# Kernel optimization log

Hardware: AMD Instinct MI355X
Metric: run time of the kernel (lower is better)

The kernel has to match this reference:

```python
import jax, jax.numpy as jnp
import numpy as np

T, N, D = 64, 40, 4
H, R, K = 256, 64, 2
E = N * (N - 1)


def _xavier(key, shape):
    std = (2.0 / (shape[0] + shape[1])) ** 0.5
    return (std * jax.random.normal(key, shape)).astype(jnp.float32)


def setup_inputs() -> dict:
    ks = iter(jax.random.split(jax.random.key(0), 40))
    send, recv = np.where(np.ones((N, N)) - np.eye(N))  # fully-connected directed graph, E = N*(N-1)
    p = {}
    p['inputs'] = jax.random.normal(next(ks), (1, T, N, D), dtype=jnp.float32)
    p['node_masks'] = jnp.ones((1, T, N), dtype=jnp.float32)
    p['send_edges'] = jnp.asarray(send, dtype=jnp.int32)
    p['recv_edges'] = jnp.asarray(recv, dtype=jnp.int32)
    for name, nin in (('mlp1', D), ('mlp2', 2 * H), ('mlp3', H), ('mlp4', 3 * H)):
        p[name + '_W1'] = _xavier(next(ks), (H, nin))
        p[name + '_b1'] = jnp.full((H,), 0.1, jnp.float32)
        p[name + '_W2'] = _xavier(next(ks), (H, H))
        p[name + '_b2'] = jnp.full((H,), 0.1, jnp.float32)
    s = float(1.0 / np.sqrt(R))
    for nm in ('fwd', 'rev'):
        p[nm + '_Wih'] = jax.random.uniform(next(ks), (4 * R, H), jnp.float32, -s, s)
        p[nm + '_Whh'] = jax.random.uniform(next(ks), (4 * R, R), jnp.float32, -s, s)
        p[nm + '_bih'] = jnp.zeros((4 * R,), jnp.float32)
        p[nm + '_bhh'] = jnp.zeros((4 * R,), jnp.float32)
    p['enc_W'] = _xavier(next(ks), (K, 2 * R))
    p['enc_b'] = jnp.full((K,), 0.1, jnp.float32)
    p['prior_W'] = _xavier(next(ks), (K, R))
    p['prior_b'] = jnp.full((K,), 0.1, jnp.float32)
    return p


def _mlp(x, W1, b1, W2, b2):
    # RefNRIMLP in eval mode with no_bn=True: elu(fc2(elu(fc1(x))))
    return jax.nn.elu(jax.nn.elu(x @ W1.T + b1) @ W2.T + b2)


def _lstm(xs, Wih, Whh, bih, bhh):
    # xs: [T, E, H] -> hidden states [T, E, R]; PyTorch LSTM gate order i, f, g, o
    def step(carry, xt):
        h, c = carry
        g = xt @ Wih.T + bih + h @ Whh.T + bhh
        i, f, gg, o = jnp.split(g, 4, axis=-1)
        c = jax.nn.sigmoid(f) * c + jax.nn.sigmoid(i) * jnp.tanh(gg)
        h = jax.nn.sigmoid(o) * jnp.tanh(c)
        return (h, c), h
    Rh = Whh.shape[1]
    init = (jnp.zeros((xs.shape[1], Rh), xs.dtype), jnp.zeros((xs.shape[1], Rh), xs.dtype))
    _, hs = jax.lax.scan(step, init, xs)
    return hs


def _encode(inputs, send, recv,
            m1W1, m1b1, m1W2, m1b2, m2W1, m2b1, m2W2, m2b2,
            m3W1, m3b1, m3W2, m3b2, m4W1, m4b1, m4W2, m4b2,
            fWih, fWhh, fbih, fbhh, rWih, rWhh, rbih, rbhh,
            encW, encb, priW, prib):
    x = inputs[0]                                                  # [T, N, D]
    h = _mlp(x, m1W1, m1b1, m1W2, m1b2)                            # [T, N, H]
    e = jnp.concatenate([h[:, send], h[:, recv]], axis=-1)         # node2edge gather [T, E, 2H]
    e = _mlp(e, m2W1, m2b1, m2W2, m2b2)                            # [T, E, H]
    skip = e
    n = jnp.zeros((x.shape[0], x.shape[1], e.shape[-1]), e.dtype)
    n = n.at[:, recv].add(e)                                       # edge2node scatter-add (index_add_)
    n = _mlp(n, m3W1, m3b1, m3W2, m3b2)                            # [T, N, H]
    e = jnp.concatenate([n[:, send], n[:, recv], skip], axis=-1)   # [T, E, 3H]
    e = _mlp(e, m4W1, m4b1, m4W2, m4b2)                            # per-edge features over time [T, E, H]
    fwd_h = _lstm(e, fWih, fWhh, fbih, fbhh)                       # [T, E, R]
    rev_h = _lstm(e[::-1], rWih, rWhh, rbih, rbhh)[::-1]           # [T, E, R]
    prior = fwd_h @ priW.T + prib                                  # [T, E, K]
    enc = jnp.concatenate([fwd_h, rev_h], axis=-1) @ encW.T + encb # [T, E, K]
    return jnp.concatenate([prior, enc], axis=-1)                  # [T, E, 2K]


def reference(inputs, node_masks, send_edges, recv_edges,
              mlp1_W1, mlp1_b1, mlp1_W2, mlp1_b2,
              mlp2_W1, mlp2_b1, mlp2_W2, mlp2_b2,
              mlp3_W1, mlp3_b1, mlp3_W2, mlp3_b2,
              mlp4_W1, mlp4_b1, mlp4_W2, mlp4_b2,
              fwd_Wih, fwd_Whh, fwd_bih, fwd_bhh,
              rev_Wih, rev_Whh, rev_bih, rev_bhh,
              enc_W, enc_b, prior_W, prior_b):
    del node_masks  # all nodes present -> static fully-connected graph each step
    return _encode(inputs, send_edges, recv_edges,
                   mlp1_W1, mlp1_b1, mlp1_W2, mlp1_b2,
                   mlp2_W1, mlp2_b1, mlp2_W2, mlp2_b2,
                   mlp3_W1, mlp3_b1, mlp3_W2, mlp3_b2,
                   mlp4_W1, mlp4_b1, mlp4_W2, mlp4_b2,
                   fwd_Wih, fwd_Whh, fwd_bih, fwd_bhh,
                   rev_Wih, rev_Whh, rev_bih, rev_bhh,
                   enc_W, enc_b, prior_W, prior_b)
```

## Files before the change

kernel.cpp:

```cpp
#include <hip/hip_runtime.h>
#include <math.h>

#define T_ 64
#define N_ 40
#define D_ 4
#define H_ 256
#define R_ 64
#define E_ 1560
#define TE_ (T_*E_)
#define TN_ (T_*N_)

typedef unsigned short us;
typedef short short8 __attribute__((ext_vector_type(8)));
typedef float f32x4 __attribute__((ext_vector_type(4)));

__device__ __forceinline__ float elu_f(float x){ return x > 0.f ? x : (__expf(x) - 1.f); }
__device__ __forceinline__ float sig_f(float x){ return 1.f/(1.f+__expf(-x)); }
__device__ __forceinline__ float tanh_f(float x){ return 2.f/(1.f+__expf(-2.f*x)) - 1.f; }
__device__ __forceinline__ float dot4(float4 a, float4 b){ return a.x*b.x + a.y*b.y + a.z*b.z + a.w*b.w; }

__device__ __forceinline__ float bf2f(us u){ return __uint_as_float(((unsigned int)u) << 16); }
__device__ __forceinline__ us f2bf(float f){
    unsigned int u = __float_as_uint(f);
    u += 0x7FFFu + ((u >> 16) & 1u);
    return (us)(u >> 16);
}
__device__ __forceinline__ float4 ld4f(const float* p){ return *(const float4*)p; }
__device__ __forceinline__ float4 ld4f(const us* p){
    ushort4 v = *(const ushort4*)p;
    return make_float4(bf2f(v.x), bf2f(v.y), bf2f(v.z), bf2f(v.w));
}
__device__ __forceinline__ void st4f(float* p, float4 v){ *(float4*)p = v; }
__device__ __forceinline__ void st4f(us* p, float4 v){
    ushort4 o; o.x = f2bf(v.x); o.y = f2bf(v.y); o.z = f2bf(v.z); o.w = f2bf(v.w);
    *(ushort4*)p = o;
}

__device__ __forceinline__ void gld16(void* lds, const void* g){
    __builtin_amdgcn_global_load_lds((const __attribute__((address_space(1))) unsigned int*)g,
                                     (__attribute__((address_space(3))) unsigned int*)lds,
                                     16, 0, 0);
}

__device__ __forceinline__ void wsplit1(const float* W, us* hi, us* lo, int i){
    const float w = W[i];
    const us h = f2bf(w);
    hi[i] = h;
    lo[i] = f2bf(w - bf2f(h));
}

__global__ __launch_bounds__(256)
void wsplit_all(const float* __restrict__ s0, us* h0, us* l0,
                const float* __restrict__ s1, us* h1, us* l1,
                const float* __restrict__ s2, us* h2, us* l2,
                const float* __restrict__ s3, us* h3, us* l3,
                const float* __restrict__ s4, us* h4, us* l4,
                const float* __restrict__ s5, us* h5, us* l5,
                const float* __restrict__ s6, us* h6, us* l6,
                const float* __restrict__ s7, us* h7, us* l7)
{
    int i = blockIdx.x * 256 + threadIdx.x;
    if (i < 131072) { wsplit1(s0, h0, l0, i); return; } i -= 131072;
    if (i <  65536) { wsplit1(s1, h1, l1, i); return; } i -=  65536;
    if (i < 196608) { wsplit1(s2, h2, l2, i); return; } i -= 196608;
    if (i <  65536) { wsplit1(s3, h3, l3, i); return; } i -=  65536;
    if (i <  65536) { wsplit1(s4, h4, l4, i); return; } i -=  65536;
    if (i <  65536) { wsplit1(s5, h5, l5, i); return; } i -=  65536;
    if (i <  16384) { wsplit1(s6, h6, l6, i); return; } i -=  16384;
    wsplit1(s7, h7, l7, i);
}

__global__ __launch_bounds__(256)
void mlp1_kernel(const float* __restrict__ x,
                 const float* __restrict__ W1, const float* __restrict__ b1,
                 const float* __restrict__ W2, const float* __restrict__ b2,
                 us* __restrict__ hout)
{
    __shared__ float xs[8][4];
    __shared__ float h1[8][256];
    const int tid = threadIdx.x;
    const int r0  = blockIdx.x * 8;

    if (tid < 32) xs[tid >> 2][tid & 3] = x[r0 * 4 + tid];
    __syncthreads();

    const float4 w1 = *(const float4*)&W1[tid * 4];
    const float bb1 = b1[tid];
    #pragma unroll
    for (int row = 0; row < 8; ++row) {
        float v = bb1 + xs[row][0]*w1.x + xs[row][1]*w1.y + xs[row][2]*w1.z + xs[row][3]*w1.w;
        h1[row][tid] = elu_f(v);
    }
    __syncthreads();

    float acc[8];
    const float bb2 = b2[tid];
    #pragma unroll
    for (int row = 0; row < 8; ++row) acc[row] = bb2;
    const float* w2row = W2 + (size_t)tid * 256;
    for (int k4 = 0; k4 < 64; ++k4) {
        const float4 w = *(const float4*)&w2row[k4 * 4];
        #pragma unroll
        for (int row = 0; row < 8; ++row) {
            const float4 hh = *(const float4*)&h1[row][k4 * 4];
            acc[row] += dot4(hh, w);
        }
    }
    #pragma unroll
    for (int row = 0; row < 8; ++row)
        hout[(size_t)(r0 + row) * 256 + tid] = f2bf(elu_f(acc[row]));
}

template<int MODE, bool DOELU>
__global__ __launch_bounds__(256)
void gemm_mfma(const us* __restrict__ A, const us* __restrict__ A2, const us* __restrict__ A3,
               const us* __restrict__ Whi, const us* __restrict__ Wlo,
               const float* __restrict__ bias1, const float* __restrict__ bias2,
               const int* __restrict__ send, const int* __restrict__ recv,
               us* __restrict__ C, int Kdim,
               const us* __restrict__ Whi2, const us* __restrict__ Wlo2,
               const float* __restrict__ bias1b, const float* __restrict__ bias2b,
               us* __restrict__ C2)
{
    __shared__ char smem[49152];

    const int tid  = threadIdx.x;
    const int lane = tid & 63;
    const int w    = tid >> 6;
    const int ml   = lane & 15;
    const int q    = lane >> 4;
    const int bx   = blockIdx.x;
    int by         = blockIdx.y;
    const int eh   = w >> 1;
    const int fh   = w & 1;

    if (MODE == 0 && C2 != nullptr && by >= 2) {
        Whi = Whi2; Wlo = Wlo2; bias1 = bias1b; bias2 = bias2b; C = C2; by -= 2;
    }

    const int srow0 = w * 32 + (lane >> 2);
    const int srow1 = srow0 + 16;
    const int cofs  = (((lane & 3) ^ ((lane >> 3) & 3)) * 8);

    const int gr0 = bx * 128 + srow0, gr1 = bx * 128 + srow1;
    const us *pA0a=nullptr,*pA1a=nullptr,*pA2a=nullptr;
    const us *pA0b=nullptr,*pA1b=nullptr,*pA2b=nullptr;
    if (MODE == 0) {
        pA0a = A + (size_t)gr0 * Kdim;
        pA0b = A + (size_t)gr1 * Kdim;
    } else {
        const int t0 = gr0 / E_, e0 = gr0 - t0 * E_;
        const int t1 = gr1 / E_, e1 = gr1 - t1 * E_;
        pA0a = A  + ((size_t)(t0 * N_ + send[e0])) * H_;
        pA1a = A2 + ((size_t)(t0 * N_ + recv[e0])) * H_;
        pA0b = A  + ((size_t)(t1 * N_ + send[e1])) * H_;
        pA1b = A2 + ((size_t)(t1 * N_ + recv[e1])) * H_;
        if (MODE == 2) { pA2a = A3 + (size_t)gr0 * H_; pA2b = A3 + (size_t)gr1 * H_; }
    }
    const us* pWh0 = Whi + (size_t)(by * 128 + srow0) * Kdim;
    const us* pWh1 = Whi + (size_t)(by * 128 + srow1) * Kdim;
    const us* pWl0 = Wlo + (size_t)(by * 128 + srow0) * Kdim;
    const us* pWl1 = Wlo + (size_t)(by * 128 + srow1) * Kdim;

    f32x4 acc[4][4];
    #pragma unroll
    for (int i = 0; i < 4; ++i)
        #pragma unroll
        for (int j = 0; j < 4; ++j)
            acc[i][j] = (f32x4){0.f, 0.f, 0.f, 0.f};

    auto stage = [&](int k0, char* base) {
        const us *sa, *sb;
        if (MODE == 0) { sa = pA0a + k0; sb = pA0b + k0; }
        else if (MODE == 1) {
            sa = (k0 < 256) ? pA0a + k0 : pA1a + (k0 - 256);
            sb = (k0 < 256) ? pA0b + k0 : pA1b + (k0 - 256);
        } else {
            sa = (k0 < 256) ? pA0a + k0 : (k0 < 512) ? pA1a + (k0 - 256) : pA2a + (k0 - 512);
            sb = (k0 < 256) ? pA0b + k0 : (k0 < 512) ? pA1b + (k0 - 256) : pA2b + (k0 - 512);
        }
        gld16(base + w * 2048,                sa + cofs);
        gld16(base + w * 2048 + 1024,         sb + cofs);
        gld16(base + 8192  + w * 2048,        pWh0 + k0 + cofs);
        gld16(base + 8192  + w * 2048 + 1024, pWh1 + k0 + cofs);
        gld16(base + 16384 + w * 2048,        pWl0 + k0 + cofs);
        gld16(base + 16384 + w * 2048 + 1024, pWl1 + k0 + cofs);
    };

    const int qs16 = (q ^ ((ml >> 1) & 3)) * 16;

    stage(0, smem);
    const int nk = Kdim >> 5;
    for (int k = 0; k < nk; ++k) {
        char* cur = smem + (k & 1) * 24576;
        char* nxt = smem + ((k + 1) & 1) * 24576;
        __builtin_amdgcn_s_barrier();
        if (k + 1 < nk) {
            stage((k + 1) * 32, nxt);
            __builtin_amdgcn_s_waitcnt(0x3F76);
        } else {
            __builtin_amdgcn_s_waitcnt(0x3F70);
        }
        __builtin_amdgcn_s_barrier();

        short8 wh[4], wl[4], ef[4];
        #pragma unroll
        for (int mt = 0; mt < 4; ++mt) {
            const int blkOf = (fh * 4 + mt) * 1024 + ml * 64 + qs16;
            wh[mt] = *(const short8*)(cur + 8192  + blkOf);
            wl[mt] = *(const short8*)(cur + 16384 + blkOf);
        }
        #pragma unroll
        for (int nt = 0; nt < 4; ++nt) {
            const int blkOf = (eh * 4 + nt) * 1024 + ml * 64 + qs16;
            ef[nt] = *(const short8*)(cur + blkOf);
        }
        #pragma unroll
        for (int mt = 0; mt < 4; ++mt)
            #pragma unroll
            for (int nt = 0; nt < 4; ++nt) {
                acc[mt][nt] = __builtin_amdgcn_mfma_f32_16x16x32_bf16(wh[mt], ef[nt], acc[mt][nt], 0, 0, 0);
                acc[mt][nt] = __builtin_amdgcn_mfma_f32_16x16x32_bf16(wl[mt], ef[nt], acc[mt][nt], 0, 0, 0);
            }
    }

    #pragma unroll
    for (int mt = 0; mt < 4; ++mt) {
        const int colb = by * 128 + fh * 64 + mt * 16 + q * 4;
        float4 bb = *(const float4*)(bias1 + colb);
        if (bias2) {
            const float4 b2 = *(const float4*)(bias2 + colb);
            bb.x += b2.x; bb.y += b2.y; bb.z += b2.z; bb.w += b2.w;
        }
        #pragma unroll
        for (int nt = 0; nt < 4; ++nt) {
            const int row = bx * 128 + eh * 64 + nt * 16 + ml;
            float4 v;
            v.x = acc[mt][nt][0] + bb.x; v.y = acc[mt][nt][1] + bb.y;
            v.z = acc[mt][nt][2] + bb.z; v.w = acc[mt][nt][3] + bb.w;
            if (DOELU) { v.x = elu_f(v.x); v.y = elu_f(v.y); v.z = elu_f(v.z); v.w = elu_f(v.w); }
            ushort4 o; o.x = f2bf(v.x); o.y = f2bf(v.y); o.z = f2bf(v.z); o.w = f2bf(v.w);
            *(ushort4*)(C + (size_t)row * 256 + colb) = o;
        }
    }
}

template<bool DOELU, typename TA, typename TC>
__global__ __launch_bounds__(256)
void gemm_nt(const TA* __restrict__ A, const float* __restrict__ W,
             const float* __restrict__ bias1,
             TC* __restrict__ C, int M, int Kdim)
{
    __shared__ float As[16][64];
    __shared__ float Ws[16][64];

    const int tid = threadIdx.x;
    const int am  = tid >> 2;
    const int ak  = (tid & 3) * 4;
    const int gm  = blockIdx.x * 64 + am;

    const TA* aptr0 = A + (size_t)gm * Kdim;
    const float* wptr = W + (size_t)(blockIdx.y * 64 + am) * Kdim;

    const int tx = tid & 15, ty = tid >> 4;
    float acc[4][4] = {};

    for (int k0 = 0; k0 < Kdim; k0 += 16) {
        const float4 a4 = ld4f(aptr0 + k0 + ak);
        const float4 w4 = *(const float4*)(wptr + k0 + (tid & 3) * 4);

        __syncthreads();
        As[ak+0][am] = a4.x; As[ak+1][am] = a4.y; As[ak+2][am] = a4.z; As[ak+3][am] = a4.w;
        const int wk = (tid & 3) * 4;
        Ws[wk+0][am] = w4.x; Ws[wk+1][am] = w4.y; Ws[wk+2][am] = w4.z; Ws[wk+3][am] = w4.w;
        __syncthreads();

        #pragma unroll
        for (int kq = 0; kq < 16; ++kq) {
            const float4 av = *(const float4*)&As[kq][ty * 4];
            const float4 wv = *(const float4*)&Ws[kq][tx * 4];
            const float a_[4] = {av.x, av.y, av.z, av.w};
            const float w_[4] = {wv.x, wv.y, wv.z, wv.w};
            #pragma unroll
            for (int i = 0; i < 4; ++i)
                #pragma unroll
                for (int j = 0; j < 4; ++j)
                    acc[i][j] += a_[i] * w_[j];
        }
    }

    const int gn = blockIdx.y * 64 + tx * 4;
    const float4 bb = *(const float4*)&bias1[gn];
    #pragma unroll
    for (int i = 0; i < 4; ++i) {
        const int row = blockIdx.x * 64 + ty * 4 + i;
        float4 o;
        o.x = acc[i][0] + bb.x; o.y = acc[i][1] + bb.y;
        o.z = acc[i][2] + bb.z; o.w = acc[i][3] + bb.w;
        if (DOELU) { o.x = elu_f(o.x); o.y = elu_f(o.y); o.z = elu_f(o.z); o.w = elu_f(o.w); }
        st4f(C + (size_t)row * 256 + gn, o);
    }
}

__global__ __launch_bounds__(256)
void aggregate_kernel(const us* __restrict__ eSkip, const int* __restrict__ recv,
                      float* __restrict__ nAgg)
{
    const int t = blockIdx.x / N_;
    const int j = blockIdx.x - t * N_;
    const int c = threadIdx.x;
    const us* basep = eSkip + (size_t)t * E_ * H_ + c;
    float acc = 0.f;
    #pragma unroll
    for (int s = 0; s < N_; ++s) {
        if (s == j) continue;
        const int e = s * (N_ - 1) + (j < s ? j : j - 1);
        acc += bf2f(basep[(size_t)e * H_]);
    }
    nAgg[(size_t)blockIdx.x * H_ + c] = acc;
}

__global__ __launch_bounds__(256)
void lstm_mfma(const us* __restrict__ Gf, const us* __restrict__ Gr,
               const us* __restrict__ fWhhH, const us* __restrict__ fWhhL,
               const us* __restrict__ rWhhH, const us* __restrict__ rWhhL,
               float* __restrict__ hsF, float* __restrict__ hsR)
{
    const int NBD = (E_ + 15) / 16;
    const bool revd = (int)blockIdx.x >= NBD;
    const int blk = revd ? (int)blockIdx.x - NBD : (int)blockIdx.x;
    const int e0 = blk * 16;
    const us* G  = revd ? Gr : Gf;
    const us* WH = revd ? rWhhH : fWhhH;
    const us* WL = revd ? rWhhL : fWhhL;
    float* hs    = revd ? hsR : hsF;

    const int tid  = threadIdx.x;
    const int lane = tid & 63;
    const int w    = tid >> 6;
    const int ml   = lane & 15;
    const int q    = lane >> 4;

    __shared__ us hHi[2][16][72];
    __shared__ us hLo[2][16][72];

    short8 wfh[4][2], wfl[4][2];
    #pragma unroll
    for (int mt = 0; mt < 4; ++mt) {
        const int row = mt * 64 + w * 16 + ml;
        #pragma unroll
        for (int ks = 0; ks < 2; ++ks) {
            wfh[mt][ks] = *(const short8*)(WH + (size_t)row * 64 + ks * 32 + q * 8);
            wfl[mt][ks] = *(const short8*)(WL + (size_t)row * 64 + ks * 32 + q * 8);
        }
    }

    for (int i = tid; i < 16 * 72; i += 256) { (&hHi[0][0][0])[i] = 0; (&hLo[0][0][0])[i] = 0; }

    const int eMF = min(e0 + ml, E_ - 1);
    const bool wr = (e0 + ml) < E_;
    const int gOfs = w * 16 + q * 4;
    float4 cst = make_float4(0.f, 0.f, 0.f, 0.f);

    ushort4 gcur[4], gnxt[4];
    {
        const int tt0 = revd ? (T_ - 1) : 0;
        const us* gp = G + ((size_t)tt0 * E_ + eMF) * 256 + gOfs;
        #pragma unroll
        for (int mt = 0; mt < 4; ++mt) gcur[mt] = *(const ushort4*)(gp + mt * 64);
    }
    __syncthreads();

    for (int s = 0; s < T_; ++s) {
        const int tt = revd ? (T_ - 1 - s) : s;
        {
            const int sn = (s + 1 < T_) ? s + 1 : s;
            const int tn = revd ? (T_ - 1 - sn) : sn;
            const us* gp = G + ((size_t)tn * E_ + eMF) * 256 + gOfs;
            #pragma unroll
            for (int mt = 0; mt < 4; ++mt) gnxt[mt] = *(const ushort4*)(gp + mt * 64);
        }
        const int rb = s & 1, wb = rb ^ 1;
        short8 bh[2], bl[2];
        #pragma unroll
        for (int ks = 0; ks < 2; ++ks) {
            bh[ks] = *(const short8*)(&hHi[rb][ml][ks * 32 + q * 8]);
            bl[ks] = *(const short8*)(&hLo[rb][ml][ks * 32 + q * 8]);
        }
        f32x4 acc[4];
        #pragma unroll
        for (int mt = 0; mt < 4; ++mt) {
            acc[mt][0] = bf2f(gcur[mt].x); acc[mt][1] = bf2f(gcur[mt].y);
            acc[mt][2] = bf2f(gcur[mt].z); acc[mt][3] = bf2f(gcur[mt].w);
            #pragma unroll
            for (int ks = 0; ks < 2; ++ks) {
                acc[mt] = __builtin_amdgcn_mfma_f32_16x16x32_bf16(wfh[mt][ks], bh[ks], acc[mt], 0, 0, 0);
                acc[mt] = __builtin_amdgcn_mfma_f32_16x16x32_bf16(wfh[mt][ks], bl[ks], acc[mt], 0, 0, 0);
                acc[mt] = __builtin_amdgcn_mfma_f32_16x16x32_bf16(wfl[mt][ks], bh[ks], acc[mt], 0, 0, 0);
            }
        }
        float4 hv;
        cst.x = sig_f(acc[1][0])*cst.x + sig_f(acc[0][0])*tanh_f(acc[2][0]); hv.x = sig_f(acc[3][0])*tanh_f(cst.x);
        cst.y = sig_f(acc[1][1])*cst.y + sig_f(acc[0][1])*tanh_f(acc[2][1]); hv.y = sig_f(acc[3][1])*tanh_f(cst.y);
        cst.z = sig_f(acc[1][2])*cst.z + sig_f(acc[0][2])*tanh_f(acc[2][2]); hv.z = sig_f(acc[3][2])*tanh_f(cst.z);
        cst.w = sig_f(acc[1][3])*cst.w + sig_f(acc[0][3])*tanh_f(acc[2][3]); hv.w = sig_f(acc[3][3])*tanh_f(cst.w);
        ushort4 hh4, hl4;
        hh4.x = f2bf(hv.x); hl4.x = f2bf(hv.x - bf2f(hh4.x));
        hh4.y = f2bf(hv.y); hl4.y = f2bf(hv.y - bf2f(hh4.y));
        hh4.z = f2bf(hv.z); hl4.z = f2bf(hv.z - bf2f(hh4.z));
        hh4.w = f2bf(hv.w); hl4.w = f2bf(hv.w - bf2f(hh4.w));
        *(ushort4*)(&hHi[wb][ml][gOfs]) = hh4;
        *(ushort4*)(&hLo[wb][ml][gOfs]) = hl4;
        if (wr)
            *(float4*)(&hs[((size_t)tt * E_ + e0 + ml) * 64 + gOfs]) = hv;
        __syncthreads();
        #pragma unroll
        for (int mt = 0; mt < 4; ++mt) gcur[mt] = gnxt[mt];
    }
}

__global__ __launch_bounds__(256)
void out_kernel(const float* __restrict__ hsF, const float* __restrict__ hsR,
                const float* __restrict__ priW, const float* __restrict__ prib,
                const float* __restrict__ encW, const float* __restrict__ encb,
                float* __restrict__ out)
{
    const int idx = blockIdx.x * 256 + threadIdx.x;
    const float* f = hsF + (size_t)idx * 64;
    const float* r = hsR + (size_t)idx * 64;
    float p0 = prib[0], p1 = prib[1], q0 = encb[0], q1 = encb[1];
    #pragma unroll
    for (int k4 = 0; k4 < 16; ++k4) {
        const float4 fv = *(const float4*)(f + k4 * 4);
        const float4 rv = *(const float4*)(r + k4 * 4);
        p0 += dot4(fv, *(const float4*)(priW + k4 * 4));
        p1 += dot4(fv, *(const float4*)(priW + 64 + k4 * 4));
        q0 += dot4(fv, *(const float4*)(encW + k4 * 4))
            + dot4(rv, *(const float4*)(encW + 64 + k4 * 4));
        q1 += dot4(fv, *(const float4*)(encW + 128 + k4 * 4))
            + dot4(rv, *(const float4*)(encW + 192 + k4 * 4));
    }
    float4 o; o.x = p0; o.y = p1; o.z = q0; o.w = q1;
    *(float4*)(out + (size_t)idx * 4) = o;
}

extern "C" void kernel_launch(void* const* d_in, const int* in_sizes, int n_in,
                              void* d_out, int out_size, void* d_ws, size_t ws_size,
                              hipStream_t stream)
{
    const float* x    = (const float*)d_in[0];
    const int*   send = (const int*)d_in[2];
    const int*   recv = (const int*)d_in[3];
    const float* m1W1 = (const float*)d_in[4];  const float* m1b1 = (const float*)d_in[5];
    const float* m1W2 = (const float*)d_in[6];  const float* m1b2 = (const float*)d_in[7];
    const float* m2W1 = (const float*)d_in[8];  const float* m2b1 = (const float*)d_in[9];
    const float* m2W2 = (const float*)d_in[10]; const float* m2b2 = (const float*)d_in[11];
    const float* m3W1 = (const float*)d_in[12]; const float* m3b1 = (const float*)d_in[13];
    const float* m3W2 = (const float*)d_in[14]; const float* m3b2 = (const float*)d_in[15];
    const float* m4W1 = (const float*)d_in[16]; const float* m4b1 = (const float*)d_in[17];
    const float* m4W2 = (const float*)d_in[18]; const float* m4b2 = (const float*)d_in[19];
    const float* fWih = (const float*)d_in[20]; const float* fWhh = (const float*)d_in[21];
    const float* fbih = (const float*)d_in[22]; const float* fbhh = (const float*)d_in[23];
    const float* rWih = (const float*)d_in[24]; const float* rWhh = (const float*)d_in[25];
    const float* rbih = (const float*)d_in[26]; const float* rbhh = (const float*)d_in[27];
    const float* encW = (const float*)d_in[28]; const float* encb = (const float*)d_in[29];
    const float* priW = (const float*)d_in[30]; const float* prib = (const float*)d_in[31];

    const size_t SZN  = (size_t)TN_ * H_;
    const size_t SZE  = (size_t)TE_ * H_;
    float* n_agg = (float*)d_ws;
    float* m3t   = n_agg + SZN;
    us* h16      = (us*)(m3t + SZN);
    us* n3       = h16 + SZN;
    us* w2aH = n3  + SZN;          us* w2aL = w2aH + 256*512;
    us* w2bH = w2aL + 256*512;     us* w2bL = w2bH + 256*256;
    us* w4aH = w2bL + 256*256;     us* w4aL = w4aH + 256*768;
    us* w4bH = w4aL + 256*768;     us* w4bL = w4bH + 256*256;
    us* wfiH = w4bL + 256*256;     us* wfiL = wfiH + 256*256;
    us* wriH = wfiL + 256*256;     us* wriL = wriH + 256*256;
    us* whfH = wriL + 256*256;     us* whfL = whfH + 256*64;
    us* whrH = whfL + 256*64;      us* whrL = whrH + 256*64;
    us* bufA16 = whrL + 256*64;
    us* bufB16 = bufA16 + SZE;
    us* bufC16 = bufB16 + SZE;
    float* hsF = (float*)bufC16;
    float* hsR = hsF + (size_t)TE_ * R_;
    const size_t needed = ((size_t)(bufC16 + SZE) - (size_t)d_ws);
    if (ws_size < needed) return;

    const dim3 gMF(TE_ / 128, 2), gMF4(TE_ / 128, 4), gN(TN_ / 64, 4);
    const us* z = nullptr; const float* zf = nullptr; us* zo = nullptr;

    wsplit_all<<<2432, 256, 0, stream>>>(m2W1, w2aH, w2aL, m2W2, w2bH, w2bL,
                                         m4W1, w4aH, w4aL, m4W2, w4bH, w4bL,
                                         fWih, wfiH, wfiL, rWih, wriH, wriL,
                                         fWhh, whfH, whfL, rWhh, whrH, whrL);

    mlp1_kernel<<<TN_ / 8, 256, 0, stream>>>(x, m1W1, m1b1, m1W2, m1b2, h16);
    gemm_mfma<1, true><<<gMF, 256, 0, stream>>>(h16, h16, nullptr, w2aH, w2aL, m2b1, nullptr, send, recv, bufA16, 512, z, z, zf, zf, zo);
    gemm_mfma<0, true><<<gMF, 256, 0, stream>>>(bufA16, nullptr, nullptr, w2bH, w2bL, m2b2, nullptr, send, recv, bufB16, 256, z, z, zf, zf, zo);
    aggregate_kernel<<<TN_, 256, 0, stream>>>(bufB16, recv, n_agg);
    gemm_nt<true, float, float><<<gN, 256, 0, stream>>>(n_agg, m3W1, m3b1, m3t, TN_, 256);
    gemm_nt<true, float, us><<<gN, 256, 0, stream>>>(m3t, m3W2, m3b2, n3, TN_, 256);
    gemm_mfma<2, true><<<gMF, 256, 0, stream>>>(n3, n3, bufB16, w4aH, w4aL, m4b1, nullptr, send, recv, bufA16, 768, z, z, zf, zf, zo);
    gemm_mfma<0, true><<<gMF, 256, 0, stream>>>(bufA16, nullptr, nullptr, w4bH, w4bL, m4b2, nullptr, send, recv, bufC16, 256, z, z, zf, zf, zo);
    gemm_mfma<0, false><<<gMF4, 256, 0, stream>>>(bufC16, nullptr, nullptr, wfiH, wfiL, fbih, fbhh, send, recv, bufA16, 256,
                                                  wriH, wriL, rbih, rbhh, bufB16);
    lstm_mfma<<<2 * ((E_ + 15) / 16), 256, 0, stream>>>(bufA16, bufB16, whfH, whfL, whrH, whrL, hsF, hsR);
    out_kernel<<<TE_ / 256, 256, 0, stream>>>(hsF, hsR, priW, prib, encW, encb, (float*)d_out);
}
```

Measured before the change: 583.5 us.

## Fuse MLP4 second layer with LSTM input-gate GEMMs via LDS-resident activations

```diff
diff --git a/kernel.cpp b/kernel.cpp
--- a/kernel.cpp
+++ b/kernel.cpp
@@ -117,12 +117,9 @@
                const us* __restrict__ Whi, const us* __restrict__ Wlo,
                const float* __restrict__ bias1, const float* __restrict__ bias2,
                const int* __restrict__ send, const int* __restrict__ recv,
-               us* __restrict__ C, int Kdim,
-               const us* __restrict__ Whi2, const us* __restrict__ Wlo2,
-               const float* __restrict__ bias1b, const float* __restrict__ bias2b,
-               us* __restrict__ C2)
-{
-    __shared__ char smem[49152];
+               us* __restrict__ C, int Kdim)
+{
+    __shared__ __align__(16) char smem[49152];
 
     const int tid  = threadIdx.x;
     const int lane = tid & 63;
@@ -130,13 +127,9 @@
     const int ml   = lane & 15;
     const int q    = lane >> 4;
     const int bx   = blockIdx.x;
-    int by         = blockIdx.y;
+    const int by   = blockIdx.y;
     const int eh   = w >> 1;
     const int fh   = w & 1;
-
-    if (MODE == 0 && C2 != nullptr && by >= 2) {
-        Whi = Whi2; Wlo = Wlo2; bias1 = bias1b; bias2 = bias2b; C = C2; by -= 2;
-    }
 
     const int srow0 = w * 32 + (lane >> 2);
     const int srow1 = srow0 + 16;
@@ -241,6 +234,145 @@
             if (DOELU) { v.x = elu_f(v.x); v.y = elu_f(v.y); v.z = elu_f(v.z); v.w = elu_f(v.w); }
             ushort4 o; o.x = f2bf(v.x); o.y = f2bf(v.y); o.z = f2bf(v.z); o.w = f2bf(v.w);
             *(ushort4*)(C + (size_t)row * 256 + colb) = o;
+        }
+    }
+}
+
+__global__ __launch_bounds__(256)
+void mlp4l2_gates(const us* __restrict__ e3,
+                  const us* __restrict__ w2H, const us* __restrict__ w2L,
+                  const float* __restrict__ b2,
+                  const us* __restrict__ fiH, const us* __restrict__ fiL,
+                  const float* __restrict__ fbih, const float* __restrict__ fbhh,
+                  const us* __restrict__ riH, const us* __restrict__ riL,
+                  const float* __restrict__ rbih, const float* __restrict__ rbhh,
+                  us* __restrict__ Gf, us* __restrict__ Gr)
+{
+    __shared__ __align__(16) us e4s[128][264];
+    __shared__ __align__(16) char stg[49152];
+
+    const int tid  = threadIdx.x;
+    const int lane = tid & 63;
+    const int w    = tid >> 6;
+    const int ml   = lane & 15;
+    const int q    = lane >> 4;
+    const int bx   = blockIdx.x;
+    const int eh   = w >> 1;
+    const int fh   = w & 1;
+
+    const int srow0 = w * 32 + (lane >> 2);
+    const int srow1 = srow0 + 16;
+    const int cofs  = (((lane & 3) ^ ((lane >> 3) & 3)) * 8);
+    const int qs16  = (q ^ ((ml >> 1) & 3)) * 16;
+
+    const us* pA0 = e3 + (size_t)(bx * 128 + srow0) * 256;
+    const us* pA1 = e3 + (size_t)(bx * 128 + srow1) * 256;
+
+    f32x4 acc[4][4];
+
+    auto seg = [&](const us* Wh, const us* Wl, int wrow, bool aLds) {
+        const us* pWh0 = Wh + (size_t)(wrow + srow0) * 256;
+        const us* pWh1 = Wh + (size_t)(wrow + srow1) * 256;
+        const us* pWl0 = Wl + (size_t)(wrow + srow0) * 256;
+        const us* pWl1 = Wl + (size_t)(wrow + srow1) * 256;
+        #pragma unroll
+        for (int i = 0; i < 4; ++i)
+            #pragma unroll
+            for (int j = 0; j < 4; ++j)
+                acc[i][j] = (f32x4){0.f, 0.f, 0.f, 0.f};
+        auto st1 = [&](int k0, char* base) {
+            if (!aLds) {
+                gld16(base + w * 2048,        pA0 + k0 + cofs);
+                gld16(base + w * 2048 + 1024, pA1 + k0 + cofs);
+            }
+            gld16(base + 8192  + w * 2048,        pWh0 + k0 + cofs);
+            gld16(base + 8192  + w * 2048 + 1024, pWh1 + k0 + cofs);
+            gld16(base + 16384 + w * 2048,        pWl0 + k0 + cofs);
+            gld16(base + 16384 + w * 2048 + 1024, pWl1 + k0 + cofs);
+        };
+        st1(0, stg);
+        for (int k = 0; k < 8; ++k) {
+            char* cur = stg + (k & 1) * 24576;
+            char* nxt = stg + ((k + 1) & 1) * 24576;
+            __builtin_amdgcn_s_barrier();
+            if (k + 1 < 8) {
+                st1((k + 1) * 32, nxt);
+                if (aLds) { __builtin_amdgcn_s_waitcnt(0x3F74); }
+                else      { __builtin_amdgcn_s_waitcnt(0x3F76); }
+            } else {
+                __builtin_amdgcn_s_waitcnt(0x3F70);
+            }
+            __builtin_amdgcn_s_barrier();
+
+            short8 wh[4], wl[4], ef[4];
+            #pragma unroll
+            for (int mt = 0; mt < 4; ++mt) {
+                const int blkOf = (fh * 4 + mt) * 1024 + ml * 64 + qs16;
+                wh[mt] = *(const short8*)(cur + 8192  + blkOf);
+                wl[mt] = *(const short8*)(cur + 16384 + blkOf);
+            }
+            #pragma unroll
+            for (int nt = 0; nt < 4; ++nt) {
+                if (aLds) {
+                    ef[nt] = *(const short8*)(&e4s[eh * 64 + nt * 16 + ml][k * 32 + q * 8]);
+                } else {
+                    const int blkOf = (eh * 4 + nt) * 1024 + ml * 64 + qs16;
+                    ef[nt] = *(const short8*)(cur + blkOf);
+                }
+            }
+            #pragma unroll
+            for (int mt = 0; mt < 4; ++mt)
+                #pragma unroll
+                for (int nt = 0; nt < 4; ++nt) {
+                    acc[mt][nt] = __builtin_amdgcn_mfma_f32_16x16x32_bf16(wh[mt], ef[nt], acc[mt][nt], 0, 0, 0);
+                    acc[mt][nt] = __builtin_amdgcn_mfma_f32_16x16x32_bf16(wl[mt], ef[nt], acc[mt][nt], 0, 0, 0);
+                }
+        }
+    };
+
+    for (int ch = 0; ch < 2; ++ch) {
+        seg(w2H, w2L, ch * 128, false);
+        #pragma unroll
+        for (int mt = 0; mt < 4; ++mt) {
+            const int colb = ch * 128 + fh * 64 + mt * 16 + q * 4;
+            const float4 bb = *(const float4*)(b2 + colb);
+            #pragma unroll
+            for (int nt = 0; nt < 4; ++nt) {
+                const int row = eh * 64 + nt * 16 + ml;
+                float4 v;
+                v.x = elu_f(acc[mt][nt][0] + bb.x); v.y = elu_f(acc[mt][nt][1] + bb.y);
+                v.z = elu_f(acc[mt][nt][2] + bb.z); v.w = elu_f(acc[mt][nt][3] + bb.w);
+                ushort4 o; o.x = f2bf(v.x); o.y = f2bf(v.y); o.z = f2bf(v.z); o.w = f2bf(v.w);
+                *(ushort4*)(&e4s[row][colb]) = o;
+            }
+        }
+    }
+    __syncthreads();
+
+    for (int dir = 0; dir < 2; ++dir) {
+        const us* WH = dir ? riH : fiH;
+        const us* WL = dir ? riL : fiL;
+        const float* bi = dir ? rbih : fbih;
+        const float* bh = dir ? rbhh : fbhh;
+        us* G = dir ? Gr : Gf;
+        for (int ch = 0; ch < 2; ++ch) {
+            seg(WH, WL, ch * 128, true);
+            #pragma unroll
+            for (int mt = 0; mt < 4; ++mt) {
+                const int colb = ch * 128 + fh * 64 + mt * 16 + q * 4;
+                float4 bb = *(const float4*)(bi + colb);
+                const float4 b2v = *(const float4*)(bh + colb);
+                bb.x += b2v.x; bb.y += b2v.y; bb.z += b2v.z; bb.w += b2v.w;
+                #pragma unroll
+                for (int nt = 0; nt < 4; ++nt) {
+                    const int row = bx * 128 + eh * 64 + nt * 16 + ml;
+                    float4 v;
+                    v.x = acc[mt][nt][0] + bb.x; v.y = acc[mt][nt][1] + bb.y;
+                    v.z = acc[mt][nt][2] + bb.z; v.w = acc[mt][nt][3] + bb.w;
+                    ushort4 o; o.x = f2bf(v.x); o.y = f2bf(v.y); o.z = f2bf(v.z); o.w = f2bf(v.w);
+                    *(ushort4*)(G + (size_t)row * 256 + colb) = o;
+                }
+            }
         }
     }
 }
@@ -488,8 +620,7 @@
     const size_t needed = ((size_t)(bufC16 + SZE) - (size_t)d_ws);
     if (ws_size < needed) return;
 
-    const dim3 gMF(TE_ / 128, 2), gMF4(TE_ / 128, 4), gN(TN_ / 64, 4);
-    const us* z = nullptr; const float* zf = nullptr; us* zo = nullptr;
+    const dim3 gMF(TE_ / 128, 2), gN(TN_ / 64, 4);
 
     wsplit_all<<<2432, 256, 0, stream>>>(m2W1, w2aH, w2aL, m2W2, w2bH, w2bL,
                                          m4W1, w4aH, w4aL, m4W2, w4bH, w4bL,
@@ -497,15 +628,16 @@
                                          fWhh, whfH, whfL, rWhh, whrH, whrL);
 
     mlp1_kernel<<<TN_ / 8, 256, 0, stream>>>(x, m1W1, m1b1, m1W2, m1b2, h16);
-    gemm_mfma<1, true><<<gMF, 256, 0, stream>>>(h16, h16, nullptr, w2aH, w2aL, m2b1, nullptr, send, recv, bufA16, 512, z, z, zf, zf, zo);
-    gemm_mfma<0, true><<<gMF, 256, 0, stream>>>(bufA16, nullptr, nullptr, w2bH, w2bL, m2b2, nullptr, send, recv, bufB16, 256, z, z, zf, zf, zo);
+    gemm_mfma<1, true><<<gMF, 256, 0, stream>>>(h16, h16, nullptr, w2aH, w2aL, m2b1, nullptr, send, recv, bufA16, 512);
+    gemm_mfma<0, true><<<gMF, 256, 0, stream>>>(bufA16, nullptr, nullptr, w2bH, w2bL, m2b2, nullptr, send, recv, bufB16, 256);
     aggregate_kernel<<<TN_, 256, 0, stream>>>(bufB16, recv, n_agg);
     gemm_nt<true, float, float><<<gN, 256, 0, stream>>>(n_agg, m3W1, m3b1, m3t, TN_, 256);
     gemm_nt<true, float, us><<<gN, 256, 0, stream>>>(m3t, m3W2, m3b2, n3, TN_, 256);
-    gemm_mfma<2, true><<<gMF, 256, 0, stream>>>(n3, n3, bufB16, w4aH, w4aL, m4b1, nullptr, send, recv, bufA16, 768, z, z, zf, zf, zo);
-    gemm_mfma<0, true><<<gMF, 256, 0, stream>>>(bufA16, nullptr, nullptr, w4bH, w4bL, m4b2, nullptr, send, recv, bufC16, 256, z, z, zf, zf, zo);
-    gemm_mfma<0, false><<<gMF4, 256, 0, stream>>>(bufC16, nullptr, nullptr, wfiH, wfiL, fbih, fbhh, send, recv, bufA16, 256,
-                                                  wriH, wriL, rbih, rbhh, bufB16);
+    gemm_mfma<2, true><<<gMF, 256, 0, stream>>>(n3, n3, bufB16, w4aH, w4aL, m4b1, nullptr, send, recv, bufA16, 768);
+    mlp4l2_gates<<<TE_ / 128, 256, 0, stream>>>(bufA16, w4bH, w4bL, m4b2,
+                                                wfiH, wfiL, fbih, fbhh,
+                                                wriH, wriL, rbih, rbhh,
+                                                bufA16, bufB16);
     lstm_mfma<<<2 * ((E_ + 15) / 16), 256, 0, stream>>>(bufA16, bufB16, whfH, whfL, whrH, whrL, hsF, hsR);
     out_kernel<<<TE_ / 256, 256, 0, stream>>>(hsF, hsR, priW, prib, encW, encb, (float*)d_out);
 }
```

Result: slower. 635.0 us (+8.8%).
